# Kernel optimization log

Measured on AMD Instinct MI355X. Metric: run time of the kernel, lower is better.

The kernel has to match this reference:

```python
import jax, jax.numpy as jnp
import numpy as np

B, T, D = 2048, 100, 128
HID = [512, 256, 128]
ALPHA, NOISE_STD = 0.2, 0.05


def _lin_init(key, fan_in, fan_out):
    k1, k2 = jax.random.split(key)
    b = 1.0 / np.sqrt(fan_in)
    W = jax.random.uniform(k1, (fan_in, fan_out), minval=-b, maxval=b, dtype=jnp.float32)
    bias = jax.random.uniform(k2, (fan_out,), minval=-b, maxval=b, dtype=jnp.float32)
    return W, bias


def setup_inputs() -> dict:
    key = jax.random.key(0)
    ks = jax.random.split(key, 10)
    x = jax.random.normal(ks[0], (B, T, D), dtype=jnp.float32)
    noise = jax.random.normal(ks[1], (B, T - 1, HID[-1]), dtype=jnp.float32)
    e_w0, e_b0 = _lin_init(ks[2], D, HID[0])
    e_w1, e_b1 = _lin_init(ks[3], HID[0], HID[1])
    e_w2, e_b2 = _lin_init(ks[4], HID[1], HID[2])
    d_w0, d_b0 = _lin_init(ks[5], HID[2], HID[1])
    d_w1, d_b1 = _lin_init(ks[6], HID[1], HID[0])
    d_w2, d_b2 = _lin_init(ks[7], HID[0], D)
    m = jax.random.normal(ks[8], (HID[-1], 2), dtype=jnp.float32)
    n = jax.random.normal(ks[9], (HID[-1], 2), dtype=jnp.float32)
    return {"x": x, "noise": noise, "seq_len": T,
            "e_w0": e_w0, "e_b0": e_b0, "e_w1": e_w1, "e_b1": e_b1,
            "e_w2": e_w2, "e_b2": e_b2, "d_w0": d_w0, "d_b0": d_b0,
            "d_w1": d_w1, "d_b1": d_b1, "d_w2": d_w2, "d_b2": d_b2,
            "m": m, "n": n}


def reference(x, noise, seq_len, e_w0, e_b0, e_w1, e_b1, e_w2, e_b2,
              d_w0, d_b0, d_w1, d_b1, d_w2, d_b2, m, n):
    hs = m.shape[0]  # latent size (128)
    x = jnp.where(jnp.isnan(x), 0.0, x)  # NaN masking as in Autoencoder.forward

    def encoder(v):
        v = jax.nn.relu(v @ e_w0 + e_b0)
        v = jax.nn.relu(v @ e_w1 + e_b1)
        return v @ e_w2 + e_b2

    def decoder(v):
        v = jax.nn.relu(v @ d_w0 + d_b0)
        v = jax.nn.relu(v @ d_w1 + d_b1)
        return v @ d_w2 + d_b2

    h_enc = encoder(x)              # (B, T, hs)
    x_reconstruct = decoder(h_enc)  # (B, T, D)
    h0 = h_enc[:, 0, :]             # (B, hs)
    x0 = x[:, 0, :]                 # (B, D)

    def step(h, nz):
        r = jnp.tanh(h)
        # low-rank recurrence: rank-2 update m n^T / hidden_size
        dh = ALPHA * (-h + (r @ n) @ m.T / hs) + NOISE_STD * nz
        h = h + dh
        out = decoder(jnp.tanh(h))
        return h, (h, out)

    _, (zs, outs) = jax.lax.scan(step, h0, jnp.swapaxes(noise, 0, 1))
    z_pred = jnp.concatenate([h0[:, None, :], jnp.swapaxes(zs, 0, 1)], axis=1)
    x_pred = jnp.concatenate([x0[:, None, :], jnp.swapaxes(outs, 0, 1)], axis=1)
    return x_pred, x_reconstruct, z_pred
```

## Files before the change

kernel.cpp:

```cpp
#include <hip/hip_runtime.h>
#include <math.h>

namespace {

constexpr int B_  = 2048;
constexpr int T_  = 100;
constexpr int D_  = 128;
constexpr int BT_ = B_ * T_;
constexpr int M_  = 64;

using f32x4  = __attribute__((ext_vector_type(4))) float;
using bf16x8 = __attribute__((ext_vector_type(8))) __bf16;

enum { MODE_ENC = 0, MODE_ID = 1, MODE_TANH = 2 };

__device__ __forceinline__ unsigned short f2bf(float f) {
  unsigned int u = __float_as_uint(f);
  return (unsigned short)((u + 0x7FFFu + ((u >> 16) & 1u)) >> 16);
}
__device__ __forceinline__ unsigned int pack2(float a, float b) {
  return (unsigned int)f2bf(a) | ((unsigned int)f2bf(b) << 16);
}
__device__ __forceinline__ float ftanh(float x) {
  const float e = __expf(2.0f * x);
  return 1.0f - 2.0f / (e + 1.0f);
}

template <int K, int NT, int KFULL>
__device__ __forceinline__ void gemm_acc(const char* __restrict__ src, const int strideB,
                                         const unsigned short* __restrict__ Wt,
                                         f32x4 (&acc)[NT][4], const int lrow, const int lk) {
  const int key = lrow << 4;
#pragma unroll
  for (int kk = 0; kk < K / 32; ++kk) {
    bf16x8 a[4];
#pragma unroll
    for (int s = 0; s < 4; ++s) {
      const int row = lrow + s * 16;
      a[s] = __builtin_bit_cast(bf16x8,
          *reinterpret_cast<const int4*>(src + row * strideB + ((kk * 64 + lk * 16) ^ key)));
    }
#pragma unroll
    for (int nt = 0; nt < NT; ++nt) {
      const bf16x8 b = __builtin_bit_cast(bf16x8,
          *reinterpret_cast<const int4*>(Wt + (size_t)(nt * 16 + lrow) * KFULL + kk * 32 + lk * 8));
#pragma unroll
      for (int s = 0; s < 4; ++s)
        acc[nt][s] = __builtin_amdgcn_mfma_f32_16x16x32_bf16(a[s], b, acc[nt][s], 0, 0, 0);
    }
  }
}

template <int NT>
__device__ __forceinline__ void init_bias(f32x4 (&acc)[NT][4], const float* __restrict__ bias,
                                          const int col0, const int lrow) {
#pragma unroll
  for (int nt = 0; nt < NT; ++nt) {
    const float bv = bias[col0 + nt * 16 + lrow];
#pragma unroll
    for (int s = 0; s < 4; ++s) acc[nt][s] = {bv, bv, bv, bv};
  }
}

template <int NT>
__device__ __forceinline__ void store_lds(char* __restrict__ dst, const int strideB,
                                          const int colLocal0, f32x4 (&acc)[NT][4],
                                          const int lrow, const int lk) {
#pragma unroll
  for (int nt = 0; nt < NT; ++nt) {
    const int col = colLocal0 + nt * 16 + lrow;
#pragma unroll
    for (int s = 0; s < 4; ++s)
#pragma unroll
      for (int j = 0; j < 4; ++j) {
        const int row = s * 16 + lk * 4 + j;
        *reinterpret_cast<unsigned short*>(dst + row * strideB + ((col * 2) ^ ((row & 15) << 4))) =
            f2bf(fmaxf(acc[nt][s][j], 0.0f));
      }
  }
}

template <int MODE>
__device__ __forceinline__ void stage(const float* __restrict__ in, char* __restrict__ X,
                                      int* __restrict__ sRow, float* __restrict__ xpred0,
                                      const int r0, const int tid) {
#pragma unroll
  for (int i = 0; i < 2; ++i) {
    const int c   = tid + i * 512;
    const int row = c >> 4;
    const int cb  = c & 15;
    const int rl  = r0 + row;
    int g;
    if constexpr (MODE == MODE_TANH) {
      const int b = rl / 99;
      g = b * T_ + (rl - b * 99) + 1;
    } else {
      g = rl;
    }
    if (cb == 0) sRow[row] = g;
    const float4* gp = reinterpret_cast<const float4*>(in + (size_t)g * 128 + cb * 8);
    float4 v0 = gp[0], v1 = gp[1];
    if constexpr (MODE == MODE_ENC) {
      v0.x = (v0.x == v0.x) ? v0.x : 0.f;  v0.y = (v0.y == v0.y) ? v0.y : 0.f;
      v0.z = (v0.z == v0.z) ? v0.z : 0.f;  v0.w = (v0.w == v0.w) ? v0.w : 0.f;
      v1.x = (v1.x == v1.x) ? v1.x : 0.f;  v1.y = (v1.y == v1.y) ? v1.y : 0.f;
      v1.z = (v1.z == v1.z) ? v1.z : 0.f;  v1.w = (v1.w == v1.w) ? v1.w : 0.f;
      if (rl % T_ == 0) {
        float4* xp = reinterpret_cast<float4*>(xpred0 + (size_t)g * 128 + cb * 8);
        xp[0] = v0; xp[1] = v1;
      }
    }
    if constexpr (MODE == MODE_TANH) {
      v0.x = ftanh(v0.x); v0.y = ftanh(v0.y); v0.z = ftanh(v0.z); v0.w = ftanh(v0.w);
      v1.x = ftanh(v1.x); v1.y = ftanh(v1.y); v1.z = ftanh(v1.z); v1.w = ftanh(v1.w);
    }
    int4 pk;
    pk.x = (int)pack2(v0.x, v0.y); pk.y = (int)pack2(v0.z, v0.w);
    pk.z = (int)pack2(v1.x, v1.y); pk.w = (int)pack2(v1.z, v1.w);
    *reinterpret_cast<int4*>(X + row * 256 + ((cb * 16) ^ ((row & 15) << 4))) = pk;
  }
}

__device__ __forceinline__ void store_global(float* __restrict__ gout, const int* __restrict__ sRow,
                                             f32x4 (&acc)[1][4], const int wave,
                                             const int lrow, const int lk) {
  const int col = wave * 16 + lrow;
#pragma unroll
  for (int s = 0; s < 4; ++s)
#pragma unroll
    for (int j = 0; j < 4; ++j) {
      const int row = s * 16 + lk * 4 + j;
      gout[(size_t)sRow[row] * 128 + col] = acc[0][s][j];
    }
}

__launch_bounds__(512, 4)
__global__ void enc_kernel(const float* __restrict__ in,
                           const unsigned short* __restrict__ W0t, const float* __restrict__ b0,
                           const unsigned short* __restrict__ W1t, const float* __restrict__ b1,
                           const unsigned short* __restrict__ W2t, const float* __restrict__ b2,
                           float* __restrict__ gout, float* __restrict__ xpred0) {
  __shared__ __align__(16) char X[M_ * 512];
  __shared__ __align__(16) char Y[M_ * 512];
  __shared__ int sRow[M_];

  const int tid  = threadIdx.x;
  const int wave = tid >> 6;
  const int lane = tid & 63;
  const int lrow = lane & 15;
  const int lk   = lane >> 4;
  const int r0   = blockIdx.x * M_;

  stage<MODE_ENC>(in, X, sRow, xpred0, r0, tid);
  __syncthreads();

  f32x4 acc2[2][4];
  init_bias<2>(acc2, b1, wave * 32, lrow);
#pragma unroll
  for (int h = 0; h < 2; ++h) {
    f32x4 acc1[2][4];
    init_bias<2>(acc1, b0, h * 256 + wave * 32, lrow);
    gemm_acc<128, 2, 128>(X, 256, W0t + (size_t)(h * 256 + wave * 32) * 128, acc1, lrow, lk);
    __syncthreads();
    store_lds<2>(Y, 512, wave * 32, acc1, lrow, lk);
    __syncthreads();
    gemm_acc<256, 2, 512>(Y, 512, W1t + (size_t)(wave * 32) * 512 + h * 256, acc2, lrow, lk);
  }
  store_lds<2>(X, 512, wave * 32, acc2, lrow, lk);
  __syncthreads();

  f32x4 acc3[1][4];
  init_bias<1>(acc3, b2, wave * 16, lrow);
  gemm_acc<256, 1, 256>(X, 512, W2t + (size_t)(wave * 16) * 256, acc3, lrow, lk);
  store_global(gout, sRow, acc3, wave, lrow, lk);
}

template <int MODE>
__launch_bounds__(512, 4)
__global__ void dec_kernel(const float* __restrict__ in,
                           const unsigned short* __restrict__ W0t, const float* __restrict__ b0,
                           const unsigned short* __restrict__ W1t, const float* __restrict__ b1,
                           const unsigned short* __restrict__ W2t, const float* __restrict__ b2,
                           float* __restrict__ gout) {
  __shared__ __align__(16) char X[M_ * 512];
  __shared__ __align__(16) char Y[M_ * 512];
  __shared__ int sRow[M_];

  const int tid  = threadIdx.x;
  const int wave = tid >> 6;
  const int lane = tid & 63;
  const int lrow = lane & 15;
  const int lk   = lane >> 4;
  const int r0   = blockIdx.x * M_;

  stage<MODE>(in, X, sRow, nullptr, r0, tid);
  __syncthreads();

  f32x4 acc1[2][4];
  init_bias<2>(acc1, b0, wave * 32, lrow);
  gemm_acc<128, 2, 128>(X, 256, W0t + (size_t)(wave * 32) * 128, acc1, lrow, lk);
  store_lds<2>(Y, 512, wave * 32, acc1, lrow, lk);
  __syncthreads();

  f32x4 acc3[1][4];
  init_bias<1>(acc3, b2, wave * 16, lrow);
#pragma unroll
  for (int h = 0; h < 2; ++h) {
    f32x4 acc2[2][4];
    init_bias<2>(acc2, b1, h * 256 + wave * 32, lrow);
    gemm_acc<256, 2, 256>(Y, 512, W1t + (size_t)(h * 256 + wave * 32) * 256, acc2, lrow, lk);
    __syncthreads();
    store_lds<2>(X, 512, wave * 32, acc2, lrow, lk);
    __syncthreads();
    gemm_acc<256, 1, 512>(X, 512, W2t + (size_t)(wave * 16) * 512 + h * 256, acc3, lrow, lk);
  }
  store_global(gout, sRow, acc3, wave, lrow, lk);
}

__global__ void wprep_kernel(const float* __restrict__ src, unsigned short* __restrict__ dst,
                             int K, int N) {
  const int id = blockIdx.x * blockDim.x + threadIdx.x;
  if (id >= K * N) return;
  const int k = id / N;
  const int n = id - k * N;
  dst[(size_t)n * K + k] = f2bf(src[id]);
}

__global__ void rnn_scan_kernel(const float* __restrict__ noise,
                                const float* __restrict__ m, const float* __restrict__ n,
                                float* __restrict__ z) {
  const int gtid = blockIdx.x * blockDim.x + threadIdx.x;
  const int b = gtid >> 6;
  const int lane = threadIdx.x & 63;
  const int k0 = lane, k1 = lane + 64;

  const float mk00 = m[k0 * 2], mk01 = m[k0 * 2 + 1];
  const float mk10 = m[k1 * 2], mk11 = m[k1 * 2 + 1];
  const float nk00 = n[k0 * 2], nk01 = n[k0 * 2 + 1];
  const float nk10 = n[k1 * 2], nk11 = n[k1 * 2 + 1];

  float* zb = z + (size_t)b * T_ * D_;
  const float* nzb = noise + (size_t)b * (T_ - 1) * D_;
  float h0 = zb[k0];
  float h1 = zb[k1];

#pragma unroll 1
  for (int t = 0; t < T_ - 1; ++t) {
    const float r0v = tanhf(h0);
    const float r1v = tanhf(h1);
    float p0 = r0v * nk00 + r1v * nk10;
    float p1 = r0v * nk01 + r1v * nk11;
#pragma unroll
    for (int off = 32; off > 0; off >>= 1) {
      p0 += __shfl_xor(p0, off);
      p1 += __shfl_xor(p1, off);
    }
    const float v0 = (p0 * mk00 + p1 * mk01) * (1.0f / 128.0f);
    const float v1 = (p0 * mk10 + p1 * mk11) * (1.0f / 128.0f);
    const float nz0 = nzb[t * D_ + k0];
    const float nz1 = nzb[t * D_ + k1];
    h0 += 0.2f * (v0 - h0) + 0.05f * nz0;
    h1 += 0.2f * (v1 - h1) + 0.05f * nz1;
    zb[(t + 1) * D_ + k0] = h0;
    zb[(t + 1) * D_ + k1] = h1;
  }
}

}

extern "C" void kernel_launch(void* const* d_in, const int* in_sizes, int n_in,
                              void* d_out, int out_size, void* d_ws, size_t ws_size,
                              hipStream_t stream) {
  (void)in_sizes; (void)n_in; (void)ws_size; (void)out_size;

  const float* x     = (const float*)d_in[0];
  const float* noise = (const float*)d_in[1];
  const float* e_w0 = (const float*)d_in[3];
  const float* e_b0 = (const float*)d_in[4];
  const float* e_w1 = (const float*)d_in[5];
  const float* e_b1 = (const float*)d_in[6];
  const float* e_w2 = (const float*)d_in[7];
  const float* e_b2 = (const float*)d_in[8];
  const float* d_w0 = (const float*)d_in[9];
  const float* d_b0 = (const float*)d_in[10];
  const float* d_w1 = (const float*)d_in[11];
  const float* d_b1 = (const float*)d_in[12];
  const float* d_w2 = (const float*)d_in[13];
  const float* d_b2 = (const float*)d_in[14];
  const float* m    = (const float*)d_in[15];
  const float* n    = (const float*)d_in[16];

  float* out    = (float*)d_out;
  float* x_pred = out;
  float* x_rec  = out + (size_t)BT_ * D_;
  float* z      = out + 2 * (size_t)BT_ * D_;

  unsigned short* ws = (unsigned short*)d_ws;
  unsigned short* eW0t = ws;
  unsigned short* eW1t = ws + 65536;
  unsigned short* eW2t = ws + 196608;
  unsigned short* dW0t = ws + 229376;
  unsigned short* dW1t = ws + 262144;
  unsigned short* dW2t = ws + 393216;

  wprep_kernel<<<(65536 + 255) / 256, 256, 0, stream>>>(e_w0, eW0t, 128, 512);
  wprep_kernel<<<(131072 + 255) / 256, 256, 0, stream>>>(e_w1, eW1t, 512, 256);
  wprep_kernel<<<(32768 + 255) / 256, 256, 0, stream>>>(e_w2, eW2t, 256, 128);
  wprep_kernel<<<(32768 + 255) / 256, 256, 0, stream>>>(d_w0, dW0t, 128, 256);
  wprep_kernel<<<(131072 + 255) / 256, 256, 0, stream>>>(d_w1, dW1t, 256, 512);
  wprep_kernel<<<(65536 + 255) / 256, 256, 0, stream>>>(d_w2, dW2t, 512, 128);

  enc_kernel<<<BT_ / M_, 512, 0, stream>>>(x, eW0t, e_b0, eW1t, e_b1, eW2t, e_b2, z, x_pred);

  dec_kernel<MODE_ID><<<BT_ / M_, 512, 0, stream>>>(z, dW0t, d_b0, dW1t, d_b1, dW2t, d_b2, x_rec);

  rnn_scan_kernel<<<B_ / 4, 256, 0, stream>>>(noise, m, n, z);

  dec_kernel<MODE_TANH><<<(B_ * (T_ - 1)) / M_, 512, 0, stream>>>(z, dW0t, d_b0, dW1t, d_b1, dW2t, d_b2, x_pred);
}
```

Measured before the change: 795.2 us.

## Fuse encoder and reconstruction decoder, coalesce output stores via LDS, merge weight prep

```diff
diff --git a/kernel.cpp b/kernel.cpp
--- a/kernel.cpp
+++ b/kernel.cpp
@@ -26,24 +26,23 @@
   return 1.0f - 2.0f / (e + 1.0f);
 }
 
-template <int K, int NT, int KFULL>
-__device__ __forceinline__ void gemm_acc(const char* __restrict__ src, const int strideB,
-                                         const unsigned short* __restrict__ Wt,
-                                         f32x4 (&acc)[NT][4], const int lrow, const int lk) {
+template <int KGEMM, int NT, int KFW>
+__device__ __forceinline__ void gemm_regB(const char* __restrict__ A, const int astr,
+                                          const unsigned short* __restrict__ Wt,
+                                          f32x4 (&acc)[NT][4], const int lrow, const int lk) {
   const int key = lrow << 4;
 #pragma unroll
-  for (int kk = 0; kk < K / 32; ++kk) {
+  for (int kk = 0; kk < KGEMM / 32; ++kk) {
     bf16x8 a[4];
 #pragma unroll
     for (int s = 0; s < 4; ++s) {
-      const int row = lrow + s * 16;
       a[s] = __builtin_bit_cast(bf16x8,
-          *reinterpret_cast<const int4*>(src + row * strideB + ((kk * 64 + lk * 16) ^ key)));
+          *reinterpret_cast<const int4*>(A + (lrow + s * 16) * astr + ((kk * 64 + lk * 16) ^ key)));
     }
 #pragma unroll
     for (int nt = 0; nt < NT; ++nt) {
-      const bf16x8 b = __builtin_bit_cast(bf16x8,
-          *reinterpret_cast<const int4*>(Wt + (size_t)(nt * 16 + lrow) * KFULL + kk * 32 + lk * 8));
+      const int4 rb = *reinterpret_cast<const int4*>(Wt + (size_t)(nt * 16 + lrow) * KFW + kk * 32 + lk * 8);
+      const bf16x8 b = __builtin_bit_cast(bf16x8, rb);
 #pragma unroll
       for (int s = 0; s < 4; ++s)
         acc[nt][s] = __builtin_amdgcn_mfma_f32_16x16x32_bf16(a[s], b, acc[nt][s], 0, 0, 0);
@@ -53,16 +52,16 @@
 
 template <int NT>
 __device__ __forceinline__ void init_bias(f32x4 (&acc)[NT][4], const float* __restrict__ bias,
-                                          const int col0, const int lrow) {
+                                          const int lrow) {
 #pragma unroll
   for (int nt = 0; nt < NT; ++nt) {
-    const float bv = bias[col0 + nt * 16 + lrow];
+    const float bv = bias[nt * 16 + lrow];
 #pragma unroll
     for (int s = 0; s < 4; ++s) acc[nt][s] = {bv, bv, bv, bv};
   }
 }
 
-template <int NT>
+template <int NT, bool RELU>
 __device__ __forceinline__ void store_lds(char* __restrict__ dst, const int strideB,
                                           const int colLocal0, f32x4 (&acc)[NT][4],
                                           const int lrow, const int lk) {
@@ -74,15 +73,49 @@
 #pragma unroll
       for (int j = 0; j < 4; ++j) {
         const int row = s * 16 + lk * 4 + j;
-        *reinterpret_cast<unsigned short*>(dst + row * strideB + ((col * 2) ^ ((row & 15) << 4))) =
-            f2bf(fmaxf(acc[nt][s][j], 0.0f));
+        const float v = RELU ? fmaxf(acc[nt][s][j], 0.0f) : acc[nt][s][j];
+        *reinterpret_cast<unsigned short*>(dst + row * strideB + ((col * 2) ^ ((row & 15) << 4))) = f2bf(v);
       }
   }
+}
+
+template <int MODE>
+__device__ __forceinline__ int rowmap(const int rl) {
+  if constexpr (MODE == MODE_TANH) {
+    const int b = rl / 99;
+    return b * T_ + (rl - b * 99) + 1;
+  }
+  return rl;
+}
+
+template <int MODE>
+__device__ __forceinline__ void bounce_out(char* __restrict__ Ybuf, float* __restrict__ gout,
+                                           f32x4 (&acc)[1][4], const int r0,
+                                           const int wave, const int lrow, const int lk,
+                                           const int tid) {
+#pragma unroll
+  for (int s = 0; s < 4; ++s)
+#pragma unroll
+    for (int j = 0; j < 4; ++j) {
+      const int row = s * 16 + lk * 4 + j;
+      *reinterpret_cast<float*>(Ybuf + row * 512 + (wave * 16 + lrow) * 4) = acc[0][s][j];
+    }
+  __syncthreads();
+#pragma unroll
+  for (int i = 0; i < 4; ++i) {
+    const int f = tid + i * 512;
+    const int r = f >> 5;
+    const int cb = f & 31;
+    const int g = rowmap<MODE>(r0 + r);
+    *reinterpret_cast<float4*>(gout + (size_t)g * D_ + cb * 4) =
+        *reinterpret_cast<const float4*>(Ybuf + r * 512 + cb * 16);
+  }
+  __syncthreads();
 }
 
 template <int MODE>
 __device__ __forceinline__ void stage(const float* __restrict__ in, char* __restrict__ X,
-                                      int* __restrict__ sRow, float* __restrict__ xpred0,
+                                      float* __restrict__ xpred0,
                                       const int r0, const int tid) {
 #pragma unroll
   for (int i = 0; i < 2; ++i) {
@@ -90,15 +123,8 @@
     const int row = c >> 4;
     const int cb  = c & 15;
     const int rl  = r0 + row;
-    int g;
-    if constexpr (MODE == MODE_TANH) {
-      const int b = rl / 99;
-      g = b * T_ + (rl - b * 99) + 1;
-    } else {
-      g = rl;
-    }
-    if (cb == 0) sRow[row] = g;
-    const float4* gp = reinterpret_cast<const float4*>(in + (size_t)g * 128 + cb * 8);
+    const int g   = rowmap<MODE>(rl);
+    const float4* gp = reinterpret_cast<const float4*>(in + (size_t)g * D_ + cb * 8);
     float4 v0 = gp[0], v1 = gp[1];
     if constexpr (MODE == MODE_ENC) {
       v0.x = (v0.x == v0.x) ? v0.x : 0.f;  v0.y = (v0.y == v0.y) ? v0.y : 0.f;
@@ -106,7 +132,7 @@
       v1.x = (v1.x == v1.x) ? v1.x : 0.f;  v1.y = (v1.y == v1.y) ? v1.y : 0.f;
       v1.z = (v1.z == v1.z) ? v1.z : 0.f;  v1.w = (v1.w == v1.w) ? v1.w : 0.f;
       if (rl % T_ == 0) {
-        float4* xp = reinterpret_cast<float4*>(xpred0 + (size_t)g * 128 + cb * 8);
+        float4* xp = reinterpret_cast<float4*>(xpred0 + (size_t)g * D_ + cb * 8);
         xp[0] = v0; xp[1] = v1;
       }
     }
@@ -121,28 +147,49 @@
   }
 }
 
-__device__ __forceinline__ void store_global(float* __restrict__ gout, const int* __restrict__ sRow,
-                                             f32x4 (&acc)[1][4], const int wave,
-                                             const int lrow, const int lk) {
-  const int col = wave * 16 + lrow;
-#pragma unroll
-  for (int s = 0; s < 4; ++s)
-#pragma unroll
-    for (int j = 0; j < 4; ++j) {
-      const int row = s * 16 + lk * 4 + j;
-      gout[(size_t)sRow[row] * 128 + col] = acc[0][s][j];
-    }
+template <int MODE>
+__device__ __forceinline__ void dec_body(const unsigned short* __restrict__ dW0t, const float* __restrict__ d_b0,
+                                         const unsigned short* __restrict__ dW1t, const float* __restrict__ d_b1,
+                                         const unsigned short* __restrict__ dW2t, const float* __restrict__ d_b2,
+                                         float* __restrict__ gout,
+                                         char* __restrict__ X, char* __restrict__ Y,
+                                         const int r0, const int wave, const int lrow, const int lk,
+                                         const int tid) {
+  f32x4 accd1[2][4];
+  init_bias<2>(accd1, d_b0 + wave * 32, lrow);
+  gemm_regB<128, 2, 128>(X, 256, dW0t + (size_t)(wave * 32) * 128, accd1, lrow, lk);
+  __syncthreads();
+  store_lds<2, true>(X, 512, wave * 32, accd1, lrow, lk);
+  __syncthreads();
+
+  f32x4 accd3[1][4];
+  init_bias<1>(accd3, d_b2 + wave * 16, lrow);
+#pragma unroll
+  for (int g = 0; g < 2; ++g) {
+    f32x4 accd2[2][4];
+    init_bias<2>(accd2, d_b1 + g * 256 + wave * 32, lrow);
+    gemm_regB<256, 2, 256>(X, 512, dW1t + (size_t)(g * 256 + wave * 32) * 256, accd2, lrow, lk);
+    __syncthreads();
+    store_lds<2, true>(Y, 512, wave * 32, accd2, lrow, lk);
+    __syncthreads();
+    gemm_regB<256, 1, 512>(Y, 512, dW2t + (size_t)(wave * 16) * 512 + g * 256, accd3, lrow, lk);
+    __syncthreads();
+  }
+  bounce_out<MODE>(Y, gout, accd3, r0, wave, lrow, lk, tid);
 }
 
 __launch_bounds__(512, 4)
-__global__ void enc_kernel(const float* __restrict__ in,
-                           const unsigned short* __restrict__ W0t, const float* __restrict__ b0,
-                           const unsigned short* __restrict__ W1t, const float* __restrict__ b1,
-                           const unsigned short* __restrict__ W2t, const float* __restrict__ b2,
-                           float* __restrict__ gout, float* __restrict__ xpred0) {
+__global__ void enc_dec_kernel(const float* __restrict__ in,
+                               const unsigned short* __restrict__ eW0t, const float* __restrict__ e_b0,
+                               const unsigned short* __restrict__ eW1t, const float* __restrict__ e_b1,
+                               const unsigned short* __restrict__ eW2t, const float* __restrict__ e_b2,
+                               const unsigned short* __restrict__ dW0t, const float* __restrict__ d_b0,
+                               const unsigned short* __restrict__ dW1t, const float* __restrict__ d_b1,
+                               const unsigned short* __restrict__ dW2t, const float* __restrict__ d_b2,
+                               float* __restrict__ z, float* __restrict__ x_rec,
+                               float* __restrict__ x_pred) {
   __shared__ __align__(16) char X[M_ * 512];
   __shared__ __align__(16) char Y[M_ * 512];
-  __shared__ int sRow[M_];
 
   const int tid  = threadIdx.x;
   const int wave = tid >> 6;
@@ -151,40 +198,44 @@
   const int lk   = lane >> 4;
   const int r0   = blockIdx.x * M_;
 
-  stage<MODE_ENC>(in, X, sRow, xpred0, r0, tid);
+  stage<MODE_ENC>(in, X, x_pred, r0, tid);
   __syncthreads();
 
   f32x4 acc2[2][4];
-  init_bias<2>(acc2, b1, wave * 32, lrow);
+  init_bias<2>(acc2, e_b1 + wave * 32, lrow);
 #pragma unroll
   for (int h = 0; h < 2; ++h) {
     f32x4 acc1[2][4];
-    init_bias<2>(acc1, b0, h * 256 + wave * 32, lrow);
-    gemm_acc<128, 2, 128>(X, 256, W0t + (size_t)(h * 256 + wave * 32) * 128, acc1, lrow, lk);
-    __syncthreads();
-    store_lds<2>(Y, 512, wave * 32, acc1, lrow, lk);
-    __syncthreads();
-    gemm_acc<256, 2, 512>(Y, 512, W1t + (size_t)(wave * 32) * 512 + h * 256, acc2, lrow, lk);
-  }
-  store_lds<2>(X, 512, wave * 32, acc2, lrow, lk);
+    init_bias<2>(acc1, e_b0 + h * 256 + wave * 32, lrow);
+    gemm_regB<128, 2, 128>(X, 256, eW0t + (size_t)(h * 256 + wave * 32) * 128, acc1, lrow, lk);
+    __syncthreads();
+    store_lds<2, true>(Y, 512, wave * 32, acc1, lrow, lk);
+    __syncthreads();
+    gemm_regB<256, 2, 512>(Y, 512, eW1t + (size_t)(wave * 32) * 512 + h * 256, acc2, lrow, lk);
+    __syncthreads();
+  }
+  store_lds<2, true>(X, 512, wave * 32, acc2, lrow, lk);
   __syncthreads();
 
   f32x4 acc3[1][4];
-  init_bias<1>(acc3, b2, wave * 16, lrow);
-  gemm_acc<256, 1, 256>(X, 512, W2t + (size_t)(wave * 16) * 256, acc3, lrow, lk);
-  store_global(gout, sRow, acc3, wave, lrow, lk);
-}
-
-template <int MODE>
+  init_bias<1>(acc3, e_b2 + wave * 16, lrow);
+  gemm_regB<256, 1, 256>(X, 512, eW2t + (size_t)(wave * 16) * 256, acc3, lrow, lk);
+  __syncthreads();
+
+  store_lds<1, false>(X, 256, wave * 16, acc3, lrow, lk);
+  bounce_out<MODE_ENC>(Y, z, acc3, r0, wave, lrow, lk, tid);
+
+  dec_body<MODE_ID>(dW0t, d_b0, dW1t, d_b1, dW2t, d_b2, x_rec, X, Y, r0, wave, lrow, lk, tid);
+}
+
 __launch_bounds__(512, 4)
-__global__ void dec_kernel(const float* __restrict__ in,
-                           const unsigned short* __restrict__ W0t, const float* __restrict__ b0,
-                           const unsigned short* __restrict__ W1t, const float* __restrict__ b1,
-                           const unsigned short* __restrict__ W2t, const float* __restrict__ b2,
-                           float* __restrict__ gout) {
+__global__ void pred_dec_kernel(const float* __restrict__ zin,
+                                const unsigned short* __restrict__ dW0t, const float* __restrict__ d_b0,
+                                const unsigned short* __restrict__ dW1t, const float* __restrict__ d_b1,
+                                const unsigned short* __restrict__ dW2t, const float* __restrict__ d_b2,
+                                float* __restrict__ x_pred) {
   __shared__ __align__(16) char X[M_ * 512];
   __shared__ __align__(16) char Y[M_ * 512];
-  __shared__ int sRow[M_];
 
   const int tid  = threadIdx.x;
   const int wave = tid >> 6;
@@ -193,37 +244,28 @@
   const int lk   = lane >> 4;
   const int r0   = blockIdx.x * M_;
 
-  stage<MODE>(in, X, sRow, nullptr, r0, tid);
-  __syncthreads();
-
-  f32x4 acc1[2][4];
-  init_bias<2>(acc1, b0, wave * 32, lrow);
-  gemm_acc<128, 2, 128>(X, 256, W0t + (size_t)(wave * 32) * 128, acc1, lrow, lk);
-  store_lds<2>(Y, 512, wave * 32, acc1, lrow, lk);
-  __syncthreads();
-
-  f32x4 acc3[1][4];
-  init_bias<1>(acc3, b2, wave * 16, lrow);
-#pragma unroll
-  for (int h = 0; h < 2; ++h) {
-    f32x4 acc2[2][4];
-    init_bias<2>(acc2, b1, h * 256 + wave * 32, lrow);
-    gemm_acc<256, 2, 256>(Y, 512, W1t + (size_t)(h * 256 + wave * 32) * 256, acc2, lrow, lk);
-    __syncthreads();
-    store_lds<2>(X, 512, wave * 32, acc2, lrow, lk);
-    __syncthreads();
-    gemm_acc<256, 1, 512>(X, 512, W2t + (size_t)(wave * 16) * 512 + h * 256, acc3, lrow, lk);
-  }
-  store_global(gout, sRow, acc3, wave, lrow, lk);
-}
-
-__global__ void wprep_kernel(const float* __restrict__ src, unsigned short* __restrict__ dst,
-                             int K, int N) {
+  stage<MODE_TANH>(zin, X, nullptr, r0, tid);
+  __syncthreads();
+  dec_body<MODE_TANH>(dW0t, d_b0, dW1t, d_b1, dW2t, d_b2, x_pred, X, Y, r0, wave, lrow, lk, tid);
+}
+
+__global__ void wprep_all_kernel(const float* __restrict__ s0, const float* __restrict__ s1,
+                                 const float* __restrict__ s2, const float* __restrict__ s3,
+                                 const float* __restrict__ s4, const float* __restrict__ s5,
+                                 unsigned short* __restrict__ d0, unsigned short* __restrict__ d1,
+                                 unsigned short* __restrict__ d2, unsigned short* __restrict__ d3,
+                                 unsigned short* __restrict__ d4, unsigned short* __restrict__ d5) {
   const int id = blockIdx.x * blockDim.x + threadIdx.x;
-  if (id >= K * N) return;
-  const int k = id / N;
-  const int n = id - k * N;
-  dst[(size_t)n * K + k] = f2bf(src[id]);
+  const float* src; unsigned short* dst; int K, N, l;
+  if (id < 65536)       { src = s0; dst = d0; K = 128; N = 512; l = id; }
+  else if (id < 196608) { src = s1; dst = d1; K = 512; N = 256; l = id - 65536; }
+  else if (id < 229376) { src = s2; dst = d2; K = 256; N = 128; l = id - 196608; }
+  else if (id < 262144) { src = s3; dst = d3; K = 128; N = 256; l = id - 229376; }
+  else if (id < 393216) { src = s4; dst = d4; K = 256; N = 512; l = id - 262144; }
+  else                  { src = s5; dst = d5; K = 512; N = 128; l = id - 393216; }
+  const int k = l / N;
+  const int n = l - k * N;
+  dst[(size_t)n * K + k] = f2bf(src[l]);
 }
 
 __global__ void rnn_scan_kernel(const float* __restrict__ noise,
@@ -303,18 +345,16 @@
   unsigned short* dW1t = ws + 262144;
   unsigned short* dW2t = ws + 393216;
 
-  wprep_kernel<<<(65536 + 255) / 256, 256, 0, stream>>>(e_w0, eW0t, 128, 512);
-  wprep_kernel<<<(131072 + 255) / 256, 256, 0, stream>>>(e_w1, eW1t, 512, 256);
-  wprep_kernel<<<(32768 + 255) / 256, 256, 0, stream>>>(e_w2, eW2t, 256, 128);
-  wprep_kernel<<<(32768 + 255) / 256, 256, 0, stream>>>(d_w0, dW0t, 128, 256);
-  wprep_kernel<<<(131072 + 255) / 256, 256, 0, stream>>>(d_w1, dW1t, 256, 512);
-  wprep_kernel<<<(65536 + 255) / 256, 256, 0, stream>>>(d_w2, dW2t, 512, 128);
-
-  enc_kernel<<<BT_ / M_, 512, 0, stream>>>(x, eW0t, e_b0, eW1t, e_b1, eW2t, e_b2, z, x_pred);
-
-  dec_kernel<MODE_ID><<<BT_ / M_, 512, 0, stream>>>(z, dW0t, d_b0, dW1t, d_b1, dW2t, d_b2, x_rec);
+  wprep_all_kernel<<<458752 / 256, 256, 0, stream>>>(e_w0, e_w1, e_w2, d_w0, d_w1, d_w2,
+                                                     eW0t, eW1t, eW2t, dW0t, dW1t, dW2t);
+
+  enc_dec_kernel<<<BT_ / M_, 512, 0, stream>>>(x,
+      eW0t, e_b0, eW1t, e_b1, eW2t, e_b2,
+      dW0t, d_b0, dW1t, d_b1, dW2t, d_b2,
+      z, x_rec, x_pred);
 
   rnn_scan_kernel<<<B_ / 4, 256, 0, stream>>>(noise, m, n, z);
 
-  dec_kernel<MODE_TANH><<<(B_ * (T_ - 1)) / M_, 512, 0, stream>>>(z, dW0t, d_b0, dW1t, d_b1, dW2t, d_b2, x_pred);
-}
+  pred_dec_kernel<<<(B_ * (T_ - 1)) / M_, 512, 0, stream>>>(z,
+      dW0t, d_b0, dW1t, d_b1, dW2t, d_b2, x_pred);
+}
```

Measured after the change: 853.2 us. 1.07x slower.
